# Kernel optimization log

Hardware: AMD Instinct MI355X
Metric: run time of the kernel (lower is better)

Reference implementation:

```python
import jax, jax.numpy as jnp
import numpy as np

BN_EPS = 1e-5


def _posit_intervals():
    # Replicates conditions_l1 / conditions_g1 interval tables (128 steps each).
    l1, g1 = [], []
    for e in range(16):
        for j in range(8):
            if j == 0:
                l1.append((0.0, 1.0625 / 2**16, 1.0 / 2**16))
            else:
                lo = (1.0625 + 0.125 * (j - 1)) / 2 ** (16 - e)
                hi = (1.0625 + 0.125 * j) / 2 ** (16 - e)
                l1.append((lo, hi, 0.5 * (lo + hi)))
            lo = (1.0625 + 0.125 * (j - 1)) * 2 ** e
            hi = (1.0625 + 0.125 * j) * 2 ** e
            g1.append((lo, hi, 0.5 * (lo + hi)))  # note: j==8 branch in torch code is dead
    return l1, g1

_L1, _G1 = _posit_intervals()


def posit_quantize(x):
    # Faithful emulation of the 128 sequential torch.where passes.
    ax = jnp.abs(x)          # conditions are fixed from the ORIGINAL tensor
    neg = x < 0
    y = x
    for (lo1, hi1, m1), (log_, hig, mg) in zip(_L1, _G1):
        c1 = jnp.logical_and(ax > lo1, ax < hi1)
        cg = jnp.logical_and(ax > log_, ax < hig)
        v1 = jnp.where(neg, -m1, m1).astype(x.dtype)
        vg = jnp.where(neg, -mg, mg).astype(x.dtype)
        # |y| < 1 gate uses the CURRENT tensor, as in the torch loop
        y = jnp.where(jnp.abs(y) < 1, jnp.where(c1, v1, y), jnp.where(cg, vg, y))
    return y


def conv1x1(x, w, b):
    # x: [N,C,D,H,W], w: [O,C] (kernel_size=1), b: [O]
    return jnp.einsum('ncdhw,oc->nodhw', x, w) + b[None, :, None, None, None]


def batchnorm(x, gamma, beta, mean, var):
    inv = gamma / jnp.sqrt(var + BN_EPS)
    return x * inv[None, :, None, None, None] + (beta - mean * inv)[None, :, None, None, None]


def setup_inputs() -> dict:
    key = jax.random.key(0)
    ks = jax.random.split(key, 12)
    C = 256
    x = jax.random.normal(ks[0], (8, C, 16, 32, 32), dtype=jnp.float32)
    w1 = jax.random.normal(ks[1], (C, C), dtype=jnp.float32) * 0.05
    b1 = jax.random.normal(ks[2], (C,), dtype=jnp.float32) * 0.05
    w2 = jax.random.normal(ks[3], (C, C), dtype=jnp.float32) * 0.05
    b2 = jax.random.normal(ks[4], (C,), dtype=jnp.float32) * 0.05
    g1 = jax.random.uniform(ks[5], (C,)) + 0.5
    be1 = jax.random.normal(ks[6], (C,)) * 0.1
    m1 = jax.random.normal(ks[7], (C,)) * 0.1
    v1 = jax.random.uniform(ks[8], (C,)) + 0.5
    g2 = jax.random.uniform(ks[9], (C,)) + 0.5
    be2 = jax.random.normal(ks[10], (C,)) * 0.1
    m2 = jax.random.normal(ks[11], (C,)) * 0.1
    v2 = jax.random.uniform(jax.random.fold_in(key, 99), (C,)) + 0.5
    return {"x": x, "w1": w1, "b1": b1, "g1": g1, "be1": be1, "m1": m1, "v1": v1,
            "w2": w2, "b2": b2, "g2": g2, "be2": be2, "m2": m2, "v2": v2}


def reference(x, w1, b1, g1, be1, m1, v1, w2, b2, g2, be2, m2, v2):
    residual = x
    out = conv1x1(posit_quantize(x), posit_quantize(w1), b1)
    out = jax.nn.relu(batchnorm(out, g1, be1, m1, v1))
    out = conv1x1(posit_quantize(out), posit_quantize(w2), b2)
    out = batchnorm(out, g2, be2, m2, v2)
    return jax.nn.relu(out + residual)
```

## Files before the change

kernel.cpp:

```cpp
#include <hip/hip_runtime.h>

typedef __attribute__((ext_vector_type(8))) short short8;
typedef __attribute__((ext_vector_type(4))) short s4v;
typedef __attribute__((ext_vector_type(4))) float floatx4;

#define SPOS 16384

__device__ __forceinline__ unsigned short f2bf(float f) {
    unsigned u = __float_as_uint(f);
    u += 0x7fffu + ((u >> 16) & 1u);
    return (unsigned short)(u >> 16);
}

__device__ __forceinline__ float posit_q(float x) {
    unsigned xu  = __float_as_uint(x);
    unsigned sgn = xu & 0x80000000u;
    unsigned au  = xu & 0x7fffffffu;
    unsigned m   = au & 0x007fffffu;
    unsigned r   = (au + 0x00080000u) & 0xfff00000u;
    bool bdry = (m & 0x000fffffu) == 0x00080000u;
    unsigned res;
    if (au >= 0x3f800000u) {
        res = r;
        if (m > 0x00700000u && m < 0x00780000u && au < 0x47700000u)
            res = (au & 0xff800000u) + 0x00800000u;
        if ((bdry && m != 0x00780000u) || au >= 0x47780000u)
            res = au;
    } else {
        res = (m <= 0x00080000u || m >= 0x00780000u || bdry) ? au : r;
        if (au < 0x37880000u) res = au ? 0x37800000u : 0u;
    }
    return __uint_as_float(sgn | res);
}

__device__ __forceinline__ float posit_q_pos(float z) {
    unsigned au  = __float_as_uint(z);
    unsigned m   = au & 0x007fffffu;
    unsigned r   = (au + 0x00080000u) & 0xfff00000u;
    bool bdry = (m & 0x000fffffu) == 0x00080000u;
    unsigned res;
    if (au >= 0x3f800000u) {
        res = r;
        if (m > 0x00700000u && m < 0x00780000u && au < 0x47700000u)
            res = (au & 0xff800000u) + 0x00800000u;
        if ((bdry && m != 0x00780000u) || au >= 0x47780000u)
            res = au;
    } else {
        res = (m <= 0x00080000u || m >= 0x00780000u || bdry) ? au : r;
        if (au < 0x37880000u) res = au ? 0x37800000u : 0u;
    }
    return __uint_as_float(res);
}

__global__ __launch_bounds__(256) void prep_kernel(
    const float* __restrict__ w1, const float* __restrict__ w2,
    const float* __restrict__ b1, const float* __restrict__ g1,
    const float* __restrict__ be1, const float* __restrict__ m1,
    const float* __restrict__ v1,
    const float* __restrict__ b2, const float* __restrict__ g2,
    const float* __restrict__ be2, const float* __restrict__ m2,
    const float* __restrict__ v2,
    unsigned short* __restrict__ w1p, unsigned short* __restrict__ w2p,
    float* __restrict__ cst)
{
    int i = blockIdx.x * 256 + threadIdx.x;
    if (i < 65536) {
        const int j    = i & 7;
        const int lane = (i >> 3) & 63;
        const int kb   = (i >> 9) & 7;
        const int G    = i >> 12;
        const int row  = 16 * G + (lane & 15);
        const int k    = 32 * kb + 8 * (lane >> 4) + j;
        w1p[i] = f2bf(posit_q(w1[row * 256 + k]));
        w2p[i] = f2bf(posit_q(w2[row * 256 + k]));
        if (i < 256) {
            float inv1 = g1[i] / sqrtf(v1[i] + 1e-5f);
            cst[i]       = inv1;
            cst[256 + i] = fmaf(b1[i], inv1, be1[i] - m1[i] * inv1);
            float inv2 = g2[i] / sqrtf(v2[i] + 1e-5f);
            cst[512 + i] = inv2;
            cst[768 + i] = fmaf(b2[i], inv2, be2[i] - m2[i] * inv2);
        }
    }
}

__device__ __forceinline__ int qidx(int p, int cb) {
    return p * 256 + ((cb ^ (p & 31)) << 3);
}

__global__ __launch_bounds__(256, 4) void fused_kernel(
    const float* __restrict__ x,
    const unsigned short* __restrict__ w1p,
    const unsigned short* __restrict__ w2p,
    const float* __restrict__ cst,
    float* __restrict__ out)
{
    __shared__ alignas(16) unsigned short q1[32 * 256];
    __shared__ alignas(16) unsigned short q2[32 * 256];

    const int b  = blockIdx.x;
    const int n  = b >> 9;
    const int s0 = (b & 511) << 5;
    const float* xb = x   + (size_t)n * (256 * SPOS) + s0;
    float*       ob = out + (size_t)n * (256 * SPOS) + s0;

    const int t    = threadIdx.x;
    const int lane = t & 63;
    const int w    = t >> 6;
    const int quad = lane >> 4;
    const int l15  = lane & 15;

    {
        const int g  = lane & 7;
        const int co = lane >> 3;
        float* xsw = (float*)q2 + w * 1024;
        const float* src0 = xb + (size_t)(64 * w + co) * SPOS + 4 * g;
        floatx4 v[8];
        #pragma unroll
        for (int r = 0; r < 8; ++r)
            v[r] = *(const floatx4*)(src0 + (size_t)(8 * r) * SPOS);
        const int p5 = lane & 31, half = lane >> 5;
        #pragma unroll
        for (int dr = 0; dr < 4; ++dr) {
            *(floatx4*)&xsw[co * 32 + 4 * (g ^ co)]       = v[2 * dr];
            *(floatx4*)&xsw[(co + 8) * 32 + 4 * (g ^ co)] = v[2 * dr + 1];
            short8 pk;
            #pragma unroll
            for (int j = 0; j < 8; ++j) {
                const int cl = 8 * half + j;
                const float val = xsw[cl * 32 + 4 * ((p5 >> 2) ^ (cl & 7)) + (p5 & 3)];
                pk[j] = (short)f2bf(posit_q(val));
            }
            *(short8*)&q1[qidx(p5, 8 * w + 2 * dr + half)] = pk;
        }
    }
    __syncthreads();

    floatx4 acc[4][2];
    #pragma unroll
    for (int i = 0; i < 4; ++i)
        #pragma unroll
        for (int jj = 0; jj < 2; ++jj)
            acc[i][jj] = (floatx4)0.0f;

    #pragma unroll
    for (int kk = 0; kk < 8; ++kk) {
        short8 af[4], bf[2];
        #pragma unroll
        for (int i = 0; i < 4; ++i)
            af[i] = *(const short8*)&w1p[(((w * 4 + i) * 8 + kk) * 64 + lane) * 8];
        #pragma unroll
        for (int jj = 0; jj < 2; ++jj)
            bf[jj] = *(const short8*)&q1[qidx(16 * jj + l15, 4 * kk + quad)];
        #pragma unroll
        for (int i = 0; i < 4; ++i)
            #pragma unroll
            for (int jj = 0; jj < 2; ++jj)
                acc[i][jj] = __builtin_amdgcn_mfma_f32_16x16x32_bf16(af[i], bf[jj], acc[i][jj], 0, 0, 0);
    }

    short8 af20[4];
    #pragma unroll
    for (int i = 0; i < 4; ++i)
        af20[i] = *(const short8*)&w2p[(((w * 4 + i) * 8 + 0) * 64 + lane) * 8];

    const int mbase = w * 64;

    {
        const float* sc1 = cst;
        const float* bi1 = cst + 256;
        #pragma unroll
        for (int i = 0; i < 4; ++i) {
            const int m0 = mbase + 16 * i + quad * 4;
            float sc[4], bi[4];
            #pragma unroll
            for (int r = 0; r < 4; ++r) { sc[r] = sc1[m0 + r]; bi[r] = bi1[m0 + r]; }
            #pragma unroll
            for (int jj = 0; jj < 2; ++jj) {
                const int p = 16 * jj + l15;
                s4v h;
                #pragma unroll
                for (int r = 0; r < 4; ++r) {
                    float z = fmaf(acc[i][jj][r], sc[r], bi[r]);
                    z = fmaxf(z, 0.0f);
                    h[r] = (short)f2bf(posit_q_pos(z));
                }
                *(s4v*)&q2[qidx(p, m0 >> 3) + (m0 & 7)] = h;
            }
        }
    }
    __syncthreads();

    #pragma unroll
    for (int i = 0; i < 4; ++i)
        #pragma unroll
        for (int jj = 0; jj < 2; ++jj)
            acc[i][jj] = (floatx4)0.0f;

    #pragma unroll
    for (int kk = 0; kk < 8; ++kk) {
        short8 af[4], bf[2];
        #pragma unroll
        for (int i = 0; i < 4; ++i)
            af[i] = (kk == 0) ? af20[i]
                  : *(const short8*)&w2p[(((w * 4 + i) * 8 + kk) * 64 + lane) * 8];
        #pragma unroll
        for (int jj = 0; jj < 2; ++jj)
            bf[jj] = *(const short8*)&q2[qidx(16 * jj + l15, 4 * kk + quad)];
        #pragma unroll
        for (int i = 0; i < 4; ++i)
            #pragma unroll
            for (int jj = 0; jj < 2; ++jj)
                acc[i][jj] = __builtin_amdgcn_mfma_f32_16x16x32_bf16(bf[jj], af[i], acc[i][jj], 0, 0, 0);
    }

    {
        const float* sc2 = cst + 512;
        const float* bi2 = cst + 768;
        float* stg = (float*)q1 + w * 1024;
        const int row_g = lane >> 3, g = lane & 7;

        floatx4 res[2][4];
        #pragma unroll
        for (int h = 0; h < 2; ++h)
            #pragma unroll
            for (int k = 0; k < 4; ++k) {
                const int ch = mbase + 32 * h + 8 * k + row_g;
                res[h][k] = *(const floatx4*)(xb + (size_t)ch * SPOS + 4 * g);
            }

        #pragma unroll
        for (int h = 0; h < 2; ++h) {
            #pragma unroll
            for (int i2 = 0; i2 < 2; ++i2) {
                const int chl = 16 * i2 + l15;
                #pragma unroll
                for (int jj = 0; jj < 2; ++jj)
                    *(floatx4*)&stg[chl * 32 + 4 * ((4 * jj + quad) ^ (chl & 7))] = acc[2 * h + i2][jj];
            }
            #pragma unroll
            for (int k = 0; k < 4; ++k) {
                const int chl = 8 * k + row_g;
                const int ch  = mbase + 32 * h + chl;
                floatx4 v = *(const floatx4*)&stg[chl * 32 + 4 * (g ^ row_g)];
                const float sc = sc2[ch];
                const float bi = bi2[ch];
                floatx4 o;
                #pragma unroll
                for (int r = 0; r < 4; ++r)
                    o[r] = fmaxf(fmaf(v[r], sc, bi) + res[h][k][r], 0.0f);
                *(floatx4*)(ob + (size_t)ch * SPOS + 4 * g) = o;
            }
        }
    }
}

extern "C" void kernel_launch(void* const* d_in, const int* in_sizes, int n_in,
                              void* d_out, int out_size, void* d_ws, size_t ws_size,
                              hipStream_t stream) {
    const float* x   = (const float*)d_in[0];
    const float* w1  = (const float*)d_in[1];
    const float* b1  = (const float*)d_in[2];
    const float* g1  = (const float*)d_in[3];
    const float* be1 = (const float*)d_in[4];
    const float* m1  = (const float*)d_in[5];
    const float* v1  = (const float*)d_in[6];
    const float* w2  = (const float*)d_in[7];
    const float* b2  = (const float*)d_in[8];
    const float* g2  = (const float*)d_in[9];
    const float* be2 = (const float*)d_in[10];
    const float* m2  = (const float*)d_in[11];
    const float* v2  = (const float*)d_in[12];

    unsigned short* w1p = (unsigned short*)d_ws;
    unsigned short* w2p = w1p + 65536;
    float* cst = (float*)(w2p + 65536);

    prep_kernel<<<256, 256, 0, stream>>>(w1, w2, b1, g1, be1, m1, v1,
                                         b2, g2, be2, m2, v2, w1p, w2p, cst);
    fused_kernel<<<4096, 256, 0, stream>>>(x, w1p, w2p, cst, (float*)d_out);
}
```

Measured before the change: 322.7 us.

## Process four spatial tiles per block with register prefetch of next input tile

After: 730.9 us. 2.26x slower.

```diff
diff --git a/kernel.cpp b/kernel.cpp
--- a/kernel.cpp
+++ b/kernel.cpp
@@ -5,6 +5,7 @@
 typedef __attribute__((ext_vector_type(4))) float floatx4;
 
 #define SPOS 16384
+#define NT 4
 
 __device__ __forceinline__ unsigned short f2bf(float f) {
     unsigned u = __float_as_uint(f);
@@ -99,159 +100,171 @@
     __shared__ alignas(16) unsigned short q2[32 * 256];
 
     const int b  = blockIdx.x;
-    const int n  = b >> 9;
-    const int s0 = (b & 511) << 5;
-    const float* xb = x   + (size_t)n * (256 * SPOS) + s0;
-    float*       ob = out + (size_t)n * (256 * SPOS) + s0;
+    const int n  = b >> 7;
+    const int p0 = (b & 127) << 7;
+    const float* xb = x   + (size_t)n * (256 * SPOS) + p0;
+    float*       ob = out + (size_t)n * (256 * SPOS) + p0;
 
     const int t    = threadIdx.x;
     const int lane = t & 63;
     const int w    = t >> 6;
     const int quad = lane >> 4;
     const int l15  = lane & 15;
-
-    {
-        const int g  = lane & 7;
-        const int co = lane >> 3;
-        float* xsw = (float*)q2 + w * 1024;
-        const float* src0 = xb + (size_t)(64 * w + co) * SPOS + 4 * g;
-        floatx4 v[8];
-        #pragma unroll
-        for (int r = 0; r < 8; ++r)
-            v[r] = *(const floatx4*)(src0 + (size_t)(8 * r) * SPOS);
-        const int p5 = lane & 31, half = lane >> 5;
-        #pragma unroll
-        for (int dr = 0; dr < 4; ++dr) {
-            *(floatx4*)&xsw[co * 32 + 4 * (g ^ co)]       = v[2 * dr];
-            *(floatx4*)&xsw[(co + 8) * 32 + 4 * (g ^ co)] = v[2 * dr + 1];
-            short8 pk;
-            #pragma unroll
-            for (int j = 0; j < 8; ++j) {
-                const int cl = 8 * half + j;
-                const float val = xsw[cl * 32 + 4 * ((p5 >> 2) ^ (cl & 7)) + (p5 & 3)];
-                pk[j] = (short)f2bf(posit_q(val));
+    const int mbase = w * 64;
+
+    const int g  = lane & 7;
+    const int co = lane >> 3;
+    const int p5 = lane & 31, half = lane >> 5;
+    const float* srcb = xb + (size_t)(64 * w + co) * SPOS + 4 * g;
+
+    floatx4 v[8];
+    #pragma unroll
+    for (int r = 0; r < 8; ++r)
+        v[r] = *(const floatx4*)(srcb + (size_t)(8 * r) * SPOS);
+
+    #pragma unroll 1
+    for (int tt = 0; tt < NT; ++tt) {
+        const int soff = 32 * tt;
+
+        {
+            float* xsw = (float*)q2 + w * 1024;
+            const float* srcn = srcb + soff + 32;
+            #pragma unroll
+            for (int dr = 0; dr < 4; ++dr) {
+                *(floatx4*)&xsw[co * 32 + 4 * (g ^ co)]       = v[2 * dr];
+                *(floatx4*)&xsw[(co + 8) * 32 + 4 * (g ^ co)] = v[2 * dr + 1];
+                if (tt + 1 < NT) {
+                    v[2 * dr]     = *(const floatx4*)(srcn + (size_t)(8 * (2 * dr)) * SPOS);
+                    v[2 * dr + 1] = *(const floatx4*)(srcn + (size_t)(8 * (2 * dr + 1)) * SPOS);
+                }
+                short8 pk;
+                #pragma unroll
+                for (int j = 0; j < 8; ++j) {
+                    const int cl = 8 * half + j;
+                    const float val = xsw[cl * 32 + 4 * ((p5 >> 2) ^ (cl & 7)) + (p5 & 3)];
+                    pk[j] = (short)f2bf(posit_q(val));
+                }
+                *(short8*)&q1[qidx(p5, 8 * w + 2 * dr + half)] = pk;
             }
-            *(short8*)&q1[qidx(p5, 8 * w + 2 * dr + half)] = pk;
-        }
-    }
-    __syncthreads();
-
-    floatx4 acc[4][2];
-    #pragma unroll
-    for (int i = 0; i < 4; ++i)
-        #pragma unroll
-        for (int jj = 0; jj < 2; ++jj)
-            acc[i][jj] = (floatx4)0.0f;
-
-    #pragma unroll
-    for (int kk = 0; kk < 8; ++kk) {
-        short8 af[4], bf[2];
+        }
+        __syncthreads();
+
+        floatx4 acc[4][2];
         #pragma unroll
         for (int i = 0; i < 4; ++i)
-            af[i] = *(const short8*)&w1p[(((w * 4 + i) * 8 + kk) * 64 + lane) * 8];
-        #pragma unroll
-        for (int jj = 0; jj < 2; ++jj)
-            bf[jj] = *(const short8*)&q1[qidx(16 * jj + l15, 4 * kk + quad)];
+            #pragma unroll
+            for (int jj = 0; jj < 2; ++jj)
+                acc[i][jj] = (floatx4)0.0f;
+
+        #pragma unroll
+        for (int kk = 0; kk < 8; ++kk) {
+            short8 af[4], bf[2];
+            #pragma unroll
+            for (int i = 0; i < 4; ++i)
+                af[i] = *(const short8*)&w1p[(((w * 4 + i) * 8 + kk) * 64 + lane) * 8];
+            #pragma unroll
+            for (int jj = 0; jj < 2; ++jj)
+                bf[jj] = *(const short8*)&q1[qidx(16 * jj + l15, 4 * kk + quad)];
+            #pragma unroll
+            for (int i = 0; i < 4; ++i)
+                #pragma unroll
+                for (int jj = 0; jj < 2; ++jj)
+                    acc[i][jj] = __builtin_amdgcn_mfma_f32_16x16x32_bf16(af[i], bf[jj], acc[i][jj], 0, 0, 0);
+        }
+
+        short8 af20[4];
         #pragma unroll
         for (int i = 0; i < 4; ++i)
-            #pragma unroll
-            for (int jj = 0; jj < 2; ++jj)
-                acc[i][jj] = __builtin_amdgcn_mfma_f32_16x16x32_bf16(af[i], bf[jj], acc[i][jj], 0, 0, 0);
-    }
-
-    short8 af20[4];
-    #pragma unroll
-    for (int i = 0; i < 4; ++i)
-        af20[i] = *(const short8*)&w2p[(((w * 4 + i) * 8 + 0) * 64 + lane) * 8];
-
-    const int mbase = w * 64;
-
-    {
-        const float* sc1 = cst;
-        const float* bi1 = cst + 256;
-        #pragma unroll
-        for (int i = 0; i < 4; ++i) {
-            const int m0 = mbase + 16 * i + quad * 4;
-            float sc[4], bi[4];
-            #pragma unroll
-            for (int r = 0; r < 4; ++r) { sc[r] = sc1[m0 + r]; bi[r] = bi1[m0 + r]; }
-            #pragma unroll
-            for (int jj = 0; jj < 2; ++jj) {
-                const int p = 16 * jj + l15;
-                s4v h;
-                #pragma unroll
-                for (int r = 0; r < 4; ++r) {
-                    float z = fmaf(acc[i][jj][r], sc[r], bi[r]);
-                    z = fmaxf(z, 0.0f);
-                    h[r] = (short)f2bf(posit_q_pos(z));
-                }
-                *(s4v*)&q2[qidx(p, m0 >> 3) + (m0 & 7)] = h;
+            af20[i] = *(const short8*)&w2p[(((w * 4 + i) * 8 + 0) * 64 + lane) * 8];
+
+        {
+            const float* sc1 = cst;
+            const float* bi1 = cst + 256;
+            #pragma unroll
+            for (int i = 0; i < 4; ++i) {
+                const int m0 = mbase + 16 * i + quad * 4;
+                float sc[4], bi[4];
+                #pragma unroll
+                for (int r = 0; r < 4; ++r) { sc[r] = sc1[m0 + r]; bi[r] = bi1[m0 + r]; }
+                #pragma unroll
+                for (int jj = 0; jj < 2; ++jj) {
+                    const int p = 16 * jj + l15;
+                    s4v h;
+                    #pragma unroll
+                    for (int r = 0; r < 4; ++r) {
+                        float z = fmaf(acc[i][jj][r], sc[r], bi[r]);
+                        z = fmaxf(z, 0.0f);
+                        h[r] = (short)f2bf(posit_q_pos(z));
+                    }
+                    *(s4v*)&q2[qidx(p, m0 >> 3) + (m0 & 7)] = h;
+                }
             }
         }
-    }
-    __syncthreads();
-
-    #pragma unroll
-    for (int i = 0; i < 4; ++i)
-        #pragma unroll
-        for (int jj = 0; jj < 2; ++jj)
-            acc[i][jj] = (floatx4)0.0f;
-
-    #pragma unroll
-    for (int kk = 0; kk < 8; ++kk) {
-        short8 af[4], bf[2];
+        __syncthreads();
+
         #pragma unroll
         for (int i = 0; i < 4; ++i)
-            af[i] = (kk == 0) ? af20[i]
-                  : *(const short8*)&w2p[(((w * 4 + i) * 8 + kk) * 64 + lane) * 8];
-        #pragma unroll
-        for (int jj = 0; jj < 2; ++jj)
-            bf[jj] = *(const short8*)&q2[qidx(16 * jj + l15, 4 * kk + quad)];
-        #pragma unroll
-        for (int i = 0; i < 4; ++i)
-            #pragma unroll
-            for (int jj = 0; jj < 2; ++jj)
-                acc[i][jj] = __builtin_amdgcn_mfma_f32_16x16x32_bf16(bf[jj], af[i], acc[i][jj], 0, 0, 0);
-    }
-
-    {
-        const float* sc2 = cst + 512;
-        const float* bi2 = cst + 768;
-        float* stg = (float*)q1 + w * 1024;
-        const int row_g = lane >> 3, g = lane & 7;
-
-        floatx4 res[2][4];
-        #pragma unroll
-        for (int h = 0; h < 2; ++h)
-            #pragma unroll
-            for (int k = 0; k < 4; ++k) {
-                const int ch = mbase + 32 * h + 8 * k + row_g;
-                res[h][k] = *(const floatx4*)(xb + (size_t)ch * SPOS + 4 * g);
+            #pragma unroll
+            for (int jj = 0; jj < 2; ++jj)
+                acc[i][jj] = (floatx4)0.0f;
+
+        #pragma unroll
+        for (int kk = 0; kk < 8; ++kk) {
+            short8 af[4], bf[2];
+            #pragma unroll
+            for (int i = 0; i < 4; ++i)
+                af[i] = (kk == 0) ? af20[i]
+                      : *(const short8*)&w2p[(((w * 4 + i) * 8 + kk) * 64 + lane) * 8];
+            #pragma unroll
+            for (int jj = 0; jj < 2; ++jj)
+                bf[jj] = *(const short8*)&q2[qidx(16 * jj + l15, 4 * kk + quad)];
+            #pragma unroll
+            for (int i = 0; i < 4; ++i)
+                #pragma unroll
+                for (int jj = 0; jj < 2; ++jj)
+                    acc[i][jj] = __builtin_amdgcn_mfma_f32_16x16x32_bf16(bf[jj], af[i], acc[i][jj], 0, 0, 0);
+        }
+
+        {
+            const float* sc2 = cst + 512;
+            const float* bi2 = cst + 768;
+            float* stg = (float*)q1 + w * 1024;
+            const int row_g = lane >> 3, ge = lane & 7;
+
+            floatx4 res[2][4];
+            #pragma unroll
+            for (int h = 0; h < 2; ++h)
+                #pragma unroll
+                for (int k = 0; k < 4; ++k) {
+                    const int ch = mbase + 32 * h + 8 * k + row_g;
+                    res[h][k] = *(const floatx4*)(xb + (size_t)ch * SPOS + soff + 4 * ge);
+                }
+
+            #pragma unroll
+            for (int h = 0; h < 2; ++h) {
+                #pragma unroll
+                for (int i2 = 0; i2 < 2; ++i2) {
+                    const int chl = 16 * i2 + l15;
+                    #pragma unroll
+                    for (int jj = 0; jj < 2; ++jj)
+                        *(floatx4*)&stg[chl * 32 + 4 * ((4 * jj + quad) ^ (chl & 7))] = acc[2 * h + i2][jj];
+                }
+                #pragma unroll
+                for (int k = 0; k < 4; ++k) {
+                    const int chl = 8 * k + row_g;
+                    const int ch  = mbase + 32 * h + chl;
+                    floatx4 vv = *(const floatx4*)&stg[chl * 32 + 4 * (ge ^ row_g)];
+                    const float sc = sc2[ch];
+                    const float bi = bi2[ch];
+                    floatx4 o;
+                    #pragma unroll
+                    for (int r = 0; r < 4; ++r)
+                        o[r] = fmaxf(fmaf(vv[r], sc, bi) + res[h][k][r], 0.0f);
+                    *(floatx4*)(ob + (size_t)ch * SPOS + soff + 4 * ge) = o;
+                }
             }
-
-        #pragma unroll
-        for (int h = 0; h < 2; ++h) {
-            #pragma unroll
-            for (int i2 = 0; i2 < 2; ++i2) {
-                const int chl = 16 * i2 + l15;
-                #pragma unroll
-                for (int jj = 0; jj < 2; ++jj)
-                    *(floatx4*)&stg[chl * 32 + 4 * ((4 * jj + quad) ^ (chl & 7))] = acc[2 * h + i2][jj];
-            }
-            #pragma unroll
-            for (int k = 0; k < 4; ++k) {
-                const int chl = 8 * k + row_g;
-                const int ch  = mbase + 32 * h + chl;
-                floatx4 v = *(const floatx4*)&stg[chl * 32 + 4 * (g ^ row_g)];
-                const float sc = sc2[ch];
-                const float bi = bi2[ch];
-                floatx4 o;
-                #pragma unroll
-                for (int r = 0; r < 4; ++r)
-                    o[r] = fmaxf(fmaf(v[r], sc, bi) + res[h][k][r], 0.0f);
-                *(floatx4*)(ob + (size_t)ch * SPOS + 4 * g) = o;
-            }
-        }
+        }
+        __syncthreads();
     }
 }
 
@@ -278,5 +291,5 @@
 
     prep_kernel<<<256, 256, 0, stream>>>(w1, w2, b1, g1, be1, m1, v1,
                                          b2, g2, be2, m2, v2, w1p, w2p, cst);
-    fused_kernel<<<4096, 256, 0, stream>>>(x, w1p, w2p, cst, (float*)d_out);
-}
+    fused_kernel<<<1024, 256, 0, stream>>>(x, w1p, w2p, cst, (float*)d_out);
+}
```
